# Kernel tuning notes

Measured on AMD Instinct MI355X. Metric: run time of the kernel, lower is better.

## Reference

```python
import jax, jax.numpy as jnp
import numpy as np

B, C, H, W = 4, 256, 64, 64
N = H * W


def setup_inputs() -> dict:
    key = jax.random.key(0)
    k1, k2, k3, k4, k5 = jax.random.split(key, 5)
    energy = jax.random.normal(k1, (B, N, N), dtype=jnp.float32)
    x = jax.random.normal(k2, (B, C, H, W), dtype=jnp.float32)
    # 1x1 conv params (kernel is [C_out, C_in] after squeezing the 1x1 spatial dims)
    fan = 1.0 / np.sqrt(C)
    value_w = jax.random.uniform(k3, (C, C), dtype=jnp.float32, minval=-fan, maxval=fan)
    value_b = jax.random.uniform(k4, (C,), dtype=jnp.float32, minval=-fan, maxval=fan)
    # nn.Parameter(torch.zeros(1)) -> use small random scalar so output is non-trivial
    gamma = jax.random.normal(k5, (1,), dtype=jnp.float32) * 0.1
    return {"energy": energy, "x": x, "value_w": value_w, "value_b": value_b, "gamma": gamma}


def reference(energy, x, value_w, value_b, gamma):
    # softmax over last dim of the [B, N, N] score matrix (dropout in eval mode = identity)
    attention = jax.nn.softmax(energy, axis=-1)  # [B, N, N]
    # 1x1 conv: per-pixel channel mixing
    value = jnp.einsum('bchw,oc->bohw', x, value_w) + value_b[None, :, None, None]
    value = value.reshape(x.shape[0], -1, N)  # [B, C, N]
    # out[b,c,m] = sum_n value[b,c,n] * attention[b,m,n]  (bmm with attention^T)
    out = jnp.einsum('bcn,bmn->bcm', value, attention)
    out = out.reshape(x.shape)  # [B, C, H, W]
    return gamma[0] * out + 2.0 * x
```

## Files before the change

### kernel.cpp

```cpp
#include <hip/hip_runtime.h>

#define Nn 4096
#define Cc 256
#define NN2 ((size_t)Nn * Nn)

typedef __attribute__((ext_vector_type(8))) short bf16x8;
typedef __attribute__((ext_vector_type(4))) float f32x4;

#define LDSBAR() do { \
    asm volatile("s_waitcnt lgkmcnt(0)" ::: "memory"); \
    __builtin_amdgcn_s_barrier(); \
} while (0)

__device__ __forceinline__ unsigned short f2bf(float f) {
    union { float f; unsigned u; } v; v.f = f;
    unsigned r = v.u + 0x7FFF + ((v.u >> 16) & 1);
    return (unsigned short)(r >> 16);
}

__device__ __forceinline__ bf16x8 pack2(const float4& a, const float4& b) {
    bf16x8 o;
    o[0] = (short)f2bf(a.x); o[1] = (short)f2bf(a.y);
    o[2] = (short)f2bf(a.z); o[3] = (short)f2bf(a.w);
    o[4] = (short)f2bf(b.x); o[5] = (short)f2bf(b.y);
    o[6] = (short)f2bf(b.z); o[7] = (short)f2bf(b.w);
    return o;
}

__device__ __forceinline__ void expstore(const float4& a, const float4& b,
                                         unsigned short* dst, float& sacc) {
    const float s0 = __expf(a.x), s1 = __expf(a.y), s2 = __expf(a.z), s3 = __expf(a.w);
    const float s4 = __expf(b.x), s5 = __expf(b.y), s6 = __expf(b.z), s7 = __expf(b.w);
    sacc += ((s0 + s1) + (s2 + s3)) + ((s4 + s5) + (s6 + s7));
    bf16x8 o;
    o[0] = (short)f2bf(s0); o[1] = (short)f2bf(s1);
    o[2] = (short)f2bf(s2); o[3] = (short)f2bf(s3);
    o[4] = (short)f2bf(s4); o[5] = (short)f2bf(s5);
    o[6] = (short)f2bf(s6); o[7] = (short)f2bf(s7);
    *(bf16x8*)dst = o;
}

__global__ __launch_bounds__(256) void value_gemm(
    const float* __restrict__ X, const float* __restrict__ W,
    const float* __restrict__ bias, unsigned short* __restrict__ Vout)
{
    __shared__ float Xs[256][33];

    const int t = threadIdx.x;
    const int b  = blockIdx.x >> 7;
    const int n0 = (blockIdx.x & 127) << 5;
    const int wave = t >> 6, lane = t & 63;
    const int lrow = lane & 15, lq = lane >> 4;

    const float* Xb = X + (size_t)b * Cc * Nn + n0;

    {
        const int r0 = t >> 3, c4 = (t & 7) << 2;
        #pragma unroll
        for (int i = 0; i < 8; ++i) {
            const int r = r0 + i * 32;
            const float4 v = *(const float4*)(Xb + (size_t)r * Nn + c4);
            Xs[r][c4 + 0] = v.x; Xs[r][c4 + 1] = v.y;
            Xs[r][c4 + 2] = v.z; Xs[r][c4 + 3] = v.w;
        }
    }
    __syncthreads();

    f32x4 acc[4][2] = {};

    #pragma unroll 2
    for (int k0 = 0; k0 < Cc; k0 += 32) {
        bf16x8 af[4];
        #pragma unroll
        for (int ci = 0; ci < 4; ++ci) {
            const float* wp = W + (size_t)(wave * 64 + ci * 16 + lrow) * Cc + k0 + lq * 8;
            af[ci] = pack2(*(const float4*)wp, *(const float4*)(wp + 4));
        }
        bf16x8 bp[2];
        #pragma unroll
        for (int mi = 0; mi < 2; ++mi) {
            const int n = mi * 16 + lrow;
            bf16x8 o;
            #pragma unroll
            for (int j = 0; j < 8; ++j) o[j] = (short)f2bf(Xs[k0 + lq * 8 + j][n]);
            bp[mi] = o;
        }
        #pragma unroll
        for (int ci = 0; ci < 4; ++ci)
            #pragma unroll
            for (int mi = 0; mi < 2; ++mi)
                acc[ci][mi] = __builtin_amdgcn_mfma_f32_16x16x32_bf16(
                    af[ci], bp[mi], acc[ci][mi], 0, 0, 0);
    }

    #pragma unroll
    for (int ci = 0; ci < 4; ++ci) {
        #pragma unroll
        for (int rr = 0; rr < 4; ++rr) {
            const int o = wave * 64 + ci * 16 + lq * 4 + rr;
            const float bo = bias[o];
            #pragma unroll
            for (int mi = 0; mi < 2; ++mi) {
                const int n = n0 + mi * 16 + lrow;
                Vout[((size_t)(b * Cc + o)) * Nn + n] = f2bf(acc[ci][mi][rr] + bo);
            }
        }
    }
}

__global__ __launch_bounds__(512) void attn_gemm(
    const unsigned short* __restrict__ V, const float* __restrict__ E,
    const float* __restrict__ X, const float* __restrict__ gamma,
    float* __restrict__ Out)
{
    __shared__ unsigned short Bbuf[2][64 * 64];
    __shared__ float sum_lds[64];

    const int t = threadIdx.x;
    const int blk = blockIdx.x;
    const int b  = blk & 3;
    const int m0 = (blk >> 2) << 6;

    const int wave = t >> 6, lane = t & 63;
    const int wm = wave >> 1, wn = wave & 1;
    const int lrow = lane & 15, lq = lane >> 4;
    const int l7 = lrow & 7;

    const int erow = t >> 3, eg = t & 7;
    const float* ep = E + (size_t)b * NN2 + (size_t)(m0 + erow) * Nn + eg * 8;
    unsigned short* const bst0 = &Bbuf[0][erow * 64 + ((eg ^ (erow & 7)) << 3)];
    unsigned short* const bst1 = &Bbuf[1][erow * 64 + ((eg ^ (erow & 7)) << 3)];

    const unsigned short* vbase = V + (size_t)(b * Cc + wm * 64) * Nn;
    int voff[4];
    #pragma unroll
    for (int ci = 0; ci < 4; ++ci) voff[ci] = (ci * 16 + lrow) * Nn + lq * 8;

    f32x4 acc[4][2] = {};
    float sacc = 0.f;

    float4 eA0, eA1, eB0, eB1;
    bf16x8 vA[8], vB[8];

    eA0 = *(const float4*)(ep);        eA1 = *(const float4*)(ep + 4);
    eB0 = *(const float4*)(ep + 64);   eB1 = *(const float4*)(ep + 68);
    #pragma unroll
    for (int kk = 0; kk < 2; ++kk)
        #pragma unroll
        for (int ci = 0; ci < 4; ++ci)
            vA[kk * 4 + ci] = *(const bf16x8*)(vbase + voff[ci] + kk * 32);
    expstore(eA0, eA1, bst0, sacc);
    eA0 = *(const float4*)(ep + 128);  eA1 = *(const float4*)(ep + 132);
    LDSBAR();

    for (int k = 0; k < 64; k += 2) {
        {
            bf16x8 bfr[2][2];
            #pragma unroll
            for (int kk = 0; kk < 2; ++kk)
                #pragma unroll
                for (int mi = 0; mi < 2; ++mi) {
                    const int rm = wn * 32 + mi * 16 + lrow;
                    bfr[kk][mi] = *(const bf16x8*)&Bbuf[0][rm * 64 + (((kk * 4 + lq) ^ l7) << 3)];
                }
            const int kv = (k + 1) << 6;
            #pragma unroll
            for (int kk = 0; kk < 2; ++kk)
                #pragma unroll
                for (int ci = 0; ci < 4; ++ci)
                    vB[kk * 4 + ci] = *(const bf16x8*)(vbase + voff[ci] + kv + kk * 32);
            expstore(eB0, eB1, bst1, sacc);
            const int ke = ((k + 3) & 63) << 6;
            eB0 = *(const float4*)(ep + ke); eB1 = *(const float4*)(ep + ke + 4);
            __builtin_amdgcn_s_setprio(1);
            #pragma unroll
            for (int ci = 0; ci < 4; ++ci)
                #pragma unroll
                for (int mi = 0; mi < 2; ++mi)
                    #pragma unroll
                    for (int kk = 0; kk < 2; ++kk)
                        acc[ci][mi] = __builtin_amdgcn_mfma_f32_16x16x32_bf16(
                            vA[kk * 4 + ci], bfr[kk][mi], acc[ci][mi], 0, 0, 0);
            __builtin_amdgcn_s_setprio(0);
            LDSBAR();
        }
        {
            bf16x8 bfr[2][2];
            #pragma unroll
            for (int kk = 0; kk < 2; ++kk)
                #pragma unroll
                for (int mi = 0; mi < 2; ++mi) {
                    const int rm = wn * 32 + mi * 16 + lrow;
                    bfr[kk][mi] = *(const bf16x8*)&Bbuf[1][rm * 64 + (((kk * 4 + lq) ^ l7) << 3)];
                }
            const int kv = ((k + 2) & 63) << 6;
            #pragma unroll
            for (int kk = 0; kk < 2; ++kk)
                #pragma unroll
                for (int ci = 0; ci < 4; ++ci)
                    vA[kk * 4 + ci] = *(const bf16x8*)(vbase + voff[ci] + kv + kk * 32);
            if (k != 62) {
                expstore(eA0, eA1, bst0, sacc);
                const int ke = ((k + 4) & 63) << 6;
                eA0 = *(const float4*)(ep + ke); eA1 = *(const float4*)(ep + ke + 4);
            }
            __builtin_amdgcn_s_setprio(1);
            #pragma unroll
            for (int ci = 0; ci < 4; ++ci)
                #pragma unroll
                for (int mi = 0; mi < 2; ++mi)
                    #pragma unroll
                    for (int kk = 0; kk < 2; ++kk)
                        acc[ci][mi] = __builtin_amdgcn_mfma_f32_16x16x32_bf16(
                            vB[kk * 4 + ci], bfr[kk][mi], acc[ci][mi], 0, 0, 0);
            __builtin_amdgcn_s_setprio(0);
            LDSBAR();
        }
    }

    {
        float s = sacc;
        s += __shfl_xor(s, 1);
        s += __shfl_xor(s, 2);
        s += __shfl_xor(s, 4);
        if (eg == 0) sum_lds[erow] = s;
    }
    LDSBAR();

    const float g = gamma[0];
    #pragma unroll
    for (int mi = 0; mi < 2; ++mi) {
        const int mloc = wn * 32 + mi * 16 + lrow;
        const float scale = g / sum_lds[mloc];
        const int m = m0 + mloc;
        #pragma unroll
        for (int ci = 0; ci < 4; ++ci) {
            #pragma unroll
            for (int rr = 0; rr < 4; ++rr) {
                const int c = wm * 64 + ci * 16 + lq * 4 + rr;
                const size_t off = ((size_t)(b * Cc + c)) * Nn + m;
                Out[off] = scale * acc[ci][mi][rr] + 2.0f * X[off];
            }
        }
    }
}

extern "C" void kernel_launch(void* const* d_in, const int* in_sizes, int n_in,
                              void* d_out, int out_size, void* d_ws, size_t ws_size,
                              hipStream_t stream) {
    const float* energy  = (const float*)d_in[0];
    const float* x       = (const float*)d_in[1];
    const float* value_w = (const float*)d_in[2];
    const float* value_b = (const float*)d_in[3];
    const float* gamma   = (const float*)d_in[4];
    float* out = (float*)d_out;
    unsigned short* Vws = (unsigned short*)d_ws;

    value_gemm<<<512, 256, 0, stream>>>(x, value_w, value_b, Vws);
    attn_gemm<<<256, 512, 0, stream>>>(Vws, energy, x, gamma, out);
}
```

Measured before the change: 451.3 us.

## Halve attention row tile to 32 to launch 512 blocks

The attention GEMM's m-tile shrinks from 64 rows to 32, which doubles the grid from 256 to 512 blocks so all CUs get work and more waves are resident. Each thread now loads one float4 of energy per step instead of two, and each wave computes one m-subtile instead of two. This cuts per-thread energy in flight and per-wave MFMA work per barrier. In exchange, the V matrix is re-read from global/L2 twice as often, and there is more barrier overhead relative to compute.

```diff
diff --git a/kernel.cpp b/kernel.cpp
--- a/kernel.cpp
+++ b/kernel.cpp
@@ -5,6 +5,7 @@
 #define NN2 ((size_t)Nn * Nn)
 
 typedef __attribute__((ext_vector_type(8))) short bf16x8;
+typedef __attribute__((ext_vector_type(4))) short bf16x4;
 typedef __attribute__((ext_vector_type(4))) float f32x4;
 
 #define LDSBAR() do { \
@@ -27,17 +28,14 @@
     return o;
 }
 
-__device__ __forceinline__ void expstore(const float4& a, const float4& b,
-                                         unsigned short* dst, float& sacc) {
+__device__ __forceinline__ void expstore4(const float4& a,
+                                          unsigned short* dst, float& sacc) {
     const float s0 = __expf(a.x), s1 = __expf(a.y), s2 = __expf(a.z), s3 = __expf(a.w);
-    const float s4 = __expf(b.x), s5 = __expf(b.y), s6 = __expf(b.z), s7 = __expf(b.w);
-    sacc += ((s0 + s1) + (s2 + s3)) + ((s4 + s5) + (s6 + s7));
-    bf16x8 o;
+    sacc += (s0 + s1) + (s2 + s3);
+    bf16x4 o;
     o[0] = (short)f2bf(s0); o[1] = (short)f2bf(s1);
     o[2] = (short)f2bf(s2); o[3] = (short)f2bf(s3);
-    o[4] = (short)f2bf(s4); o[5] = (short)f2bf(s5);
-    o[6] = (short)f2bf(s6); o[7] = (short)f2bf(s7);
-    *(bf16x8*)dst = o;
+    *(bf16x4*)dst = o;
 }
 
 __global__ __launch_bounds__(256) void value_gemm(
@@ -113,86 +111,81 @@
     const float* __restrict__ X, const float* __restrict__ gamma,
     float* __restrict__ Out)
 {
-    __shared__ unsigned short Bbuf[2][64 * 64];
-    __shared__ float sum_lds[64];
+    __shared__ unsigned short Bbuf[2][32 * 64];
+    __shared__ float sum_lds[32];
 
     const int t = threadIdx.x;
     const int blk = blockIdx.x;
     const int b  = blk & 3;
-    const int m0 = (blk >> 2) << 6;
+    const int m0 = (blk >> 2) << 5;
 
     const int wave = t >> 6, lane = t & 63;
     const int wm = wave >> 1, wn = wave & 1;
     const int lrow = lane & 15, lq = lane >> 4;
     const int l7 = lrow & 7;
 
-    const int erow = t >> 3, eg = t & 7;
-    const float* ep = E + (size_t)b * NN2 + (size_t)(m0 + erow) * Nn + eg * 8;
-    unsigned short* const bst0 = &Bbuf[0][erow * 64 + ((eg ^ (erow & 7)) << 3)];
-    unsigned short* const bst1 = &Bbuf[1][erow * 64 + ((eg ^ (erow & 7)) << 3)];
+    const int erow = t >> 4, eg = t & 15;
+    const float* ep = E + (size_t)b * NN2 + (size_t)(m0 + erow) * Nn + eg * 4;
+    const int ss = erow * 64 + ((((eg >> 1)) ^ (erow & 7)) << 3) + ((eg & 1) << 2);
+    unsigned short* const bst0 = &Bbuf[0][ss];
+    unsigned short* const bst1 = &Bbuf[1][ss];
 
     const unsigned short* vbase = V + (size_t)(b * Cc + wm * 64) * Nn;
     int voff[4];
     #pragma unroll
     for (int ci = 0; ci < 4; ++ci) voff[ci] = (ci * 16 + lrow) * Nn + lq * 8;
 
-    f32x4 acc[4][2] = {};
+    f32x4 acc[4] = {};
     float sacc = 0.f;
 
-    float4 eA0, eA1, eB0, eB1;
+    float4 eA, eB;
     bf16x8 vA[8], vB[8];
 
-    eA0 = *(const float4*)(ep);        eA1 = *(const float4*)(ep + 4);
-    eB0 = *(const float4*)(ep + 64);   eB1 = *(const float4*)(ep + 68);
+    eA = *(const float4*)(ep);
+    eB = *(const float4*)(ep + 64);
     #pragma unroll
     for (int kk = 0; kk < 2; ++kk)
         #pragma unroll
         for (int ci = 0; ci < 4; ++ci)
             vA[kk * 4 + ci] = *(const bf16x8*)(vbase + voff[ci] + kk * 32);
-    expstore(eA0, eA1, bst0, sacc);
-    eA0 = *(const float4*)(ep + 128);  eA1 = *(const float4*)(ep + 132);
+    expstore4(eA, bst0, sacc);
+    eA = *(const float4*)(ep + 128);
     LDSBAR();
 
     for (int k = 0; k < 64; k += 2) {
         {
-            bf16x8 bfr[2][2];
-            #pragma unroll
-            for (int kk = 0; kk < 2; ++kk)
-                #pragma unroll
-                for (int mi = 0; mi < 2; ++mi) {
-                    const int rm = wn * 32 + mi * 16 + lrow;
-                    bfr[kk][mi] = *(const bf16x8*)&Bbuf[0][rm * 64 + (((kk * 4 + lq) ^ l7) << 3)];
-                }
+            bf16x8 bfr[2];
+            #pragma unroll
+            for (int kk = 0; kk < 2; ++kk) {
+                const int rm = wn * 16 + lrow;
+                bfr[kk] = *(const bf16x8*)&Bbuf[0][rm * 64 + (((kk * 4 + lq) ^ l7) << 3)];
+            }
             const int kv = (k + 1) << 6;
             #pragma unroll
             for (int kk = 0; kk < 2; ++kk)
                 #pragma unroll
                 for (int ci = 0; ci < 4; ++ci)
                     vB[kk * 4 + ci] = *(const bf16x8*)(vbase + voff[ci] + kv + kk * 32);
-            expstore(eB0, eB1, bst1, sacc);
+            expstore4(eB, bst1, sacc);
             const int ke = ((k + 3) & 63) << 6;
-            eB0 = *(const float4*)(ep + ke); eB1 = *(const float4*)(ep + ke + 4);
+            eB = *(const float4*)(ep + ke);
             __builtin_amdgcn_s_setprio(1);
             #pragma unroll
             for (int ci = 0; ci < 4; ++ci)
                 #pragma unroll
-                for (int mi = 0; mi < 2; ++mi)
-                    #pragma unroll
-                    for (int kk = 0; kk < 2; ++kk)
-                        acc[ci][mi] = __builtin_amdgcn_mfma_f32_16x16x32_bf16(
-                            vA[kk * 4 + ci], bfr[kk][mi], acc[ci][mi], 0, 0, 0);
+                for (int kk = 0; kk < 2; ++kk)
+                    acc[ci] = __builtin_amdgcn_mfma_f32_16x16x32_bf16(
+                        vA[kk * 4 + ci], bfr[kk], acc[ci], 0, 0, 0);
             __builtin_amdgcn_s_setprio(0);
             LDSBAR();
         }
         {
-            bf16x8 bfr[2][2];
-            #pragma unroll
-            for (int kk = 0; kk < 2; ++kk)
-                #pragma unroll
-                for (int mi = 0; mi < 2; ++mi) {
-                    const int rm = wn * 32 + mi * 16 + lrow;
-                    bfr[kk][mi] = *(const bf16x8*)&Bbuf[1][rm * 64 + (((kk * 4 + lq) ^ l7) << 3)];
-                }
+            bf16x8 bfr[2];
+            #pragma unroll
+            for (int kk = 0; kk < 2; ++kk) {
+                const int rm = wn * 16 + lrow;
+                bfr[kk] = *(const bf16x8*)&Bbuf[1][rm * 64 + (((kk * 4 + lq) ^ l7) << 3)];
+            }
             const int kv = ((k + 2) & 63) << 6;
             #pragma unroll
             for (int kk = 0; kk < 2; ++kk)
@@ -200,19 +193,17 @@
                 for (int ci = 0; ci < 4; ++ci)
                     vA[kk * 4 + ci] = *(const bf16x8*)(vbase + voff[ci] + kv + kk * 32);
             if (k != 62) {
-                expstore(eA0, eA1, bst0, sacc);
+                expstore4(eA, bst0, sacc);
                 const int ke = ((k + 4) & 63) << 6;
-                eA0 = *(const float4*)(ep + ke); eA1 = *(const float4*)(ep + ke + 4);
+                eA = *(const float4*)(ep + ke);
             }
             __builtin_amdgcn_s_setprio(1);
             #pragma unroll
             for (int ci = 0; ci < 4; ++ci)
                 #pragma unroll
-                for (int mi = 0; mi < 2; ++mi)
-                    #pragma unroll
-                    for (int kk = 0; kk < 2; ++kk)
-                        acc[ci][mi] = __builtin_amdgcn_mfma_f32_16x16x32_bf16(
-                            vB[kk * 4 + ci], bfr[kk][mi], acc[ci][mi], 0, 0, 0);
+                for (int kk = 0; kk < 2; ++kk)
+                    acc[ci] = __builtin_amdgcn_mfma_f32_16x16x32_bf16(
+                        vB[kk * 4 + ci], bfr[kk], acc[ci], 0, 0, 0);
             __builtin_amdgcn_s_setprio(0);
             LDSBAR();
         }
@@ -223,14 +214,14 @@
         s += __shfl_xor(s, 1);
         s += __shfl_xor(s, 2);
         s += __shfl_xor(s, 4);
+        s += __shfl_xor(s, 8);
         if (eg == 0) sum_lds[erow] = s;
     }
     LDSBAR();
 
     const float g = gamma[0];
-    #pragma unroll
-    for (int mi = 0; mi < 2; ++mi) {
-        const int mloc = wn * 32 + mi * 16 + lrow;
+    {
+        const int mloc = wn * 16 + lrow;
         const float scale = g / sum_lds[mloc];
         const int m = m0 + mloc;
         #pragma unroll
@@ -239,7 +230,7 @@
             for (int rr = 0; rr < 4; ++rr) {
                 const int c = wm * 64 + ci * 16 + lq * 4 + rr;
                 const size_t off = ((size_t)(b * Cc + c)) * Nn + m;
-                Out[off] = scale * acc[ci][mi][rr] + 2.0f * X[off];
+                Out[off] = scale * acc[ci][rr] + 2.0f * X[off];
             }
         }
     }
@@ -257,5 +248,5 @@
     unsigned short* Vws = (unsigned short*)d_ws;
 
     value_gemm<<<512, 256, 0, stream>>>(x, value_w, value_b, Vws);
-    attn_gemm<<<256, 512, 0, stream>>>(Vws, energy, x, gamma, out);
-}
+    attn_gemm<<<512, 512, 0, stream>>>(Vws, energy, x, gamma, out);
+}
```

Result: slower. 551.5 us (+22.2%).

## Compute softmax exp directly in MFMA register layout, removing LDS staging and barriers

Applied to the files above, without the earlier changes.

The attention GEMM kernel no longer stages exponentiated energy tiles through shared memory. Each wave loads the energy elements matching its MFMA B-operand fragment, exponentiates and converts them to bf16 in registers, and feeds them straight into MFMA. Row sums are reduced with cross-lane shuffles. Blocks shrink to 256 threads covering 32 rows, with two blocks per CU, so every wave redundantly loads and exponentiates the same energy rows. V is also re-read by twice as many blocks.

```diff
diff --git a/kernel.cpp b/kernel.cpp
--- a/kernel.cpp
+++ b/kernel.cpp
@@ -6,11 +6,6 @@
 
 typedef __attribute__((ext_vector_type(8))) short bf16x8;
 typedef __attribute__((ext_vector_type(4))) float f32x4;
-
-#define LDSBAR() do { \
-    asm volatile("s_waitcnt lgkmcnt(0)" ::: "memory"); \
-    __builtin_amdgcn_s_barrier(); \
-} while (0)
 
 __device__ __forceinline__ unsigned short f2bf(float f) {
     union { float f; unsigned u; } v; v.f = f;
@@ -27,8 +22,7 @@
     return o;
 }
 
-__device__ __forceinline__ void expstore(const float4& a, const float4& b,
-                                         unsigned short* dst, float& sacc) {
+__device__ __forceinline__ bf16x8 exp8acc(const float4 a, const float4 b, float& sacc) {
     const float s0 = __expf(a.x), s1 = __expf(a.y), s2 = __expf(a.z), s3 = __expf(a.w);
     const float s4 = __expf(b.x), s5 = __expf(b.y), s6 = __expf(b.z), s7 = __expf(b.w);
     sacc += ((s0 + s1) + (s2 + s3)) + ((s4 + s5) + (s6 + s7));
@@ -37,7 +31,7 @@
     o[2] = (short)f2bf(s2); o[3] = (short)f2bf(s3);
     o[4] = (short)f2bf(s4); o[5] = (short)f2bf(s5);
     o[6] = (short)f2bf(s6); o[7] = (short)f2bf(s7);
-    *(bf16x8*)dst = o;
+    return o;
 }
 
 __global__ __launch_bounds__(256) void value_gemm(
@@ -108,138 +102,114 @@
     }
 }
 
-__global__ __launch_bounds__(512) void attn_gemm(
+__global__ __launch_bounds__(256, 2) void attn_gemm(
     const unsigned short* __restrict__ V, const float* __restrict__ E,
     const float* __restrict__ X, const float* __restrict__ gamma,
     float* __restrict__ Out)
 {
-    __shared__ unsigned short Bbuf[2][64 * 64];
-    __shared__ float sum_lds[64];
-
     const int t = threadIdx.x;
+    const int wave = t >> 6, lane = t & 63;
+    const int lrow = lane & 15, lq = lane >> 4;
     const int blk = blockIdx.x;
     const int b  = blk & 3;
-    const int m0 = (blk >> 2) << 6;
-
-    const int wave = t >> 6, lane = t & 63;
-    const int wm = wave >> 1, wn = wave & 1;
-    const int lrow = lane & 15, lq = lane >> 4;
-    const int l7 = lrow & 7;
-
-    const int erow = t >> 3, eg = t & 7;
-    const float* ep = E + (size_t)b * NN2 + (size_t)(m0 + erow) * Nn + eg * 8;
-    unsigned short* const bst0 = &Bbuf[0][erow * 64 + ((eg ^ (erow & 7)) << 3)];
-    unsigned short* const bst1 = &Bbuf[1][erow * 64 + ((eg ^ (erow & 7)) << 3)];
-
-    const unsigned short* vbase = V + (size_t)(b * Cc + wm * 64) * Nn;
+    const int m0 = (blk >> 2) << 5;
+    const int c0 = wave << 6;
+
+    const float* ep0 = E + (size_t)b * NN2 + (size_t)(m0 + lrow) * Nn + lq * 8;
+    const float* ep1 = ep0 + (size_t)16 * Nn;
+
+    const unsigned short* vbase = V + (size_t)(b * Cc + c0) * Nn;
     int voff[4];
     #pragma unroll
     for (int ci = 0; ci < 4; ++ci) voff[ci] = (ci * 16 + lrow) * Nn + lq * 8;
 
     f32x4 acc[4][2] = {};
-    float sacc = 0.f;
-
-    float4 eA0, eA1, eB0, eB1;
+    float sacc0 = 0.f, sacc1 = 0.f;
+
+    float4 eA[8], eB[8];
     bf16x8 vA[8], vB[8];
 
-    eA0 = *(const float4*)(ep);        eA1 = *(const float4*)(ep + 4);
-    eB0 = *(const float4*)(ep + 64);   eB1 = *(const float4*)(ep + 68);
+    #pragma unroll
+    for (int kk = 0; kk < 2; ++kk) {
+        eA[0 + kk * 2 + 0] = *(const float4*)(ep0 + kk * 32);
+        eA[0 + kk * 2 + 1] = *(const float4*)(ep0 + kk * 32 + 4);
+        eA[4 + kk * 2 + 0] = *(const float4*)(ep1 + kk * 32);
+        eA[4 + kk * 2 + 1] = *(const float4*)(ep1 + kk * 32 + 4);
+        eB[0 + kk * 2 + 0] = *(const float4*)(ep0 + 64 + kk * 32);
+        eB[0 + kk * 2 + 1] = *(const float4*)(ep0 + 64 + kk * 32 + 4);
+        eB[4 + kk * 2 + 0] = *(const float4*)(ep1 + 64 + kk * 32);
+        eB[4 + kk * 2 + 1] = *(const float4*)(ep1 + 64 + kk * 32 + 4);
+    }
     #pragma unroll
     for (int kk = 0; kk < 2; ++kk)
         #pragma unroll
-        for (int ci = 0; ci < 4; ++ci)
+        for (int ci = 0; ci < 4; ++ci) {
             vA[kk * 4 + ci] = *(const bf16x8*)(vbase + voff[ci] + kk * 32);
-    expstore(eA0, eA1, bst0, sacc);
-    eA0 = *(const float4*)(ep + 128);  eA1 = *(const float4*)(ep + 132);
-    LDSBAR();
-
+            vB[kk * 4 + ci] = *(const bf16x8*)(vbase + voff[ci] + 64 + kk * 32);
+        }
+
+#define HALF(Ee, Vv, ks)                                                      \
+    {                                                                          \
+        bf16x8 bfr00 = exp8acc(Ee[0], Ee[1], sacc0);              \
+        bf16x8 bfr01 = exp8acc(Ee[2], Ee[3], sacc0);              \
+        bf16x8 bfr10 = exp8acc(Ee[4], Ee[5], sacc1);              \
+        bf16x8 bfr11 = exp8acc(Ee[6], Ee[7], sacc1);              \
+        const int kc = (((ks) + 2) & 63) << 6;                                 \
+        Ee[0] = *(const float4*)(ep0 + kc);                                    \
+        Ee[1] = *(const float4*)(ep0 + kc + 4);                                \
+        Ee[2] = *(const float4*)(ep0 + kc + 32);                               \
+        Ee[3] = *(const float4*)(ep0 + kc + 36);                               \
+        Ee[4] = *(const float4*)(ep1 + kc);                                    \
+        Ee[5] = *(const float4*)(ep1 + kc + 4);                                \
+        Ee[6] = *(const float4*)(ep1 + kc + 32);                               \
+        Ee[7] = *(const float4*)(ep1 + kc + 36);                               \
+        _Pragma("unroll")                                                      \
+        for (int ci = 0; ci < 4; ++ci) {                                       \
+            acc[ci][0] = __builtin_amdgcn_mfma_f32_16x16x32_bf16(              \
+                Vv[ci], bfr00, acc[ci][0], 0, 0, 0);                           \
+            acc[ci][1] = __builtin_amdgcn_mfma_f32_16x16x32_bf16(              \
+                Vv[ci], bfr10, acc[ci][1], 0, 0, 0);                           \
+        }                                                                      \
+        _Pragma("unroll")                                                      \
+        for (int ci = 0; ci < 4; ++ci) {                                       \
+            acc[ci][0] = __builtin_amdgcn_mfma_f32_16x16x32_bf16(              \
+                Vv[4 + ci], bfr01, acc[ci][0], 0, 0, 0);                       \
+            acc[ci][1] = __builtin_amdgcn_mfma_f32_16x16x32_bf16(              \
+                Vv[4 + ci], bfr11, acc[ci][1], 0, 0, 0);                       \
+        }                                                                      \
+        _Pragma("unroll")                                                      \
+        for (int ci = 0; ci < 4; ++ci) {                                       \
+            Vv[ci]     = *(const bf16x8*)(vbase + voff[ci] + kc);              \
+            Vv[4 + ci] = *(const bf16x8*)(vbase + voff[ci] + kc + 32);         \
+        }                                                                      \
+    }
+
+    #pragma unroll 1
     for (int k = 0; k < 64; k += 2) {
-        {
-            bf16x8 bfr[2][2];
-            #pragma unroll
-            for (int kk = 0; kk < 2; ++kk)
-                #pragma unroll
-                for (int mi = 0; mi < 2; ++mi) {
-                    const int rm = wn * 32 + mi * 16 + lrow;
-                    bfr[kk][mi] = *(const bf16x8*)&Bbuf[0][rm * 64 + (((kk * 4 + lq) ^ l7) << 3)];
-                }
-            const int kv = (k + 1) << 6;
-            #pragma unroll
-            for (int kk = 0; kk < 2; ++kk)
-                #pragma unroll
-                for (int ci = 0; ci < 4; ++ci)
-                    vB[kk * 4 + ci] = *(const bf16x8*)(vbase + voff[ci] + kv + kk * 32);
-            expstore(eB0, eB1, bst1, sacc);
-            const int ke = ((k + 3) & 63) << 6;
-            eB0 = *(const float4*)(ep + ke); eB1 = *(const float4*)(ep + ke + 4);
-            __builtin_amdgcn_s_setprio(1);
-            #pragma unroll
-            for (int ci = 0; ci < 4; ++ci)
-                #pragma unroll
-                for (int mi = 0; mi < 2; ++mi)
-                    #pragma unroll
-                    for (int kk = 0; kk < 2; ++kk)
-                        acc[ci][mi] = __builtin_amdgcn_mfma_f32_16x16x32_bf16(
-                            vA[kk * 4 + ci], bfr[kk][mi], acc[ci][mi], 0, 0, 0);
-            __builtin_amdgcn_s_setprio(0);
-            LDSBAR();
-        }
-        {
-            bf16x8 bfr[2][2];
-            #pragma unroll
-            for (int kk = 0; kk < 2; ++kk)
-                #pragma unroll
-                for (int mi = 0; mi < 2; ++mi) {
-                    const int rm = wn * 32 + mi * 16 + lrow;
-                    bfr[kk][mi] = *(const bf16x8*)&Bbuf[1][rm * 64 + (((kk * 4 + lq) ^ l7) << 3)];
-                }
-            const int kv = ((k + 2) & 63) << 6;
-            #pragma unroll
-            for (int kk = 0; kk < 2; ++kk)
-                #pragma unroll
-                for (int ci = 0; ci < 4; ++ci)
-                    vA[kk * 4 + ci] = *(const bf16x8*)(vbase + voff[ci] + kv + kk * 32);
-            if (k != 62) {
-                expstore(eA0, eA1, bst0, sacc);
-                const int ke = ((k + 4) & 63) << 6;
-                eA0 = *(const float4*)(ep + ke); eA1 = *(const float4*)(ep + ke + 4);
-            }
-            __builtin_amdgcn_s_setprio(1);
-            #pragma unroll
-            for (int ci = 0; ci < 4; ++ci)
-                #pragma unroll
-                for (int mi = 0; mi < 2; ++mi)
-                    #pragma unroll
-                    for (int kk = 0; kk < 2; ++kk)
-                        acc[ci][mi] = __builtin_amdgcn_mfma_f32_16x16x32_bf16(
-                            vB[kk * 4 + ci], bfr[kk][mi], acc[ci][mi], 0, 0, 0);
-            __builtin_amdgcn_s_setprio(0);
-            LDSBAR();
-        }
-    }
-
-    {
-        float s = sacc;
-        s += __shfl_xor(s, 1);
-        s += __shfl_xor(s, 2);
-        s += __shfl_xor(s, 4);
-        if (eg == 0) sum_lds[erow] = s;
-    }
-    LDSBAR();
+        HALF(eA, vA, k);
+        HALF(eB, vB, k + 1);
+    }
+#undef HALF
+
+    float s0 = sacc0;
+    s0 += __shfl_xor(s0, 16);
+    s0 += __shfl_xor(s0, 32);
+    float s1 = sacc1;
+    s1 += __shfl_xor(s1, 16);
+    s1 += __shfl_xor(s1, 32);
 
     const float g = gamma[0];
+    const float sc[2] = { g / s0, g / s1 };
     #pragma unroll
     for (int mi = 0; mi < 2; ++mi) {
-        const int mloc = wn * 32 + mi * 16 + lrow;
-        const float scale = g / sum_lds[mloc];
-        const int m = m0 + mloc;
+        const int m = m0 + mi * 16 + lrow;
         #pragma unroll
         for (int ci = 0; ci < 4; ++ci) {
             #pragma unroll
             for (int rr = 0; rr < 4; ++rr) {
-                const int c = wm * 64 + ci * 16 + lq * 4 + rr;
+                const int c = c0 + ci * 16 + lq * 4 + rr;
                 const size_t off = ((size_t)(b * Cc + c)) * Nn + m;
-                Out[off] = scale * acc[ci][mi][rr] + 2.0f * X[off];
+                Out[off] = sc[mi] * acc[ci][mi][rr] + 2.0f * X[off];
             }
         }
     }
@@ -257,5 +227,5 @@
     unsigned short* Vws = (unsigned short*)d_ws;
 
     value_gemm<<<512, 256, 0, stream>>>(x, value_w, value_b, Vws);
-    attn_gemm<<<256, 512, 0, stream>>>(Vws, energy, x, gamma, out);
-}
+    attn_gemm<<<512, 256, 0, stream>>>(Vws, energy, x, gamma, out);
+}
```

After: 827.5 us. +83.4%, slower.

## Halve attention row tile to 32 rows and double grid for occupancy

Applied to the files above, without the earlier changes.

The attention GEMM now processes 32 query rows per block instead of 64, with 512 blocks instead of 256, so every CU gets work and more waves are resident (launch bounds request 4 waves per EU). Each wave covers 32 channels over all 32 rows, and the exp staging uses float4 per thread with an adjusted LDS swizzle. V is now re-read from global/L2 twice as often across blocks, and per-wave MFMA work per barrier is halved, adding sync overhead relative to compute.

```diff
diff --git a/kernel.cpp b/kernel.cpp
--- a/kernel.cpp
+++ b/kernel.cpp
@@ -5,6 +5,7 @@
 #define NN2 ((size_t)Nn * Nn)
 
 typedef __attribute__((ext_vector_type(8))) short bf16x8;
+typedef __attribute__((ext_vector_type(4))) short bf16x4;
 typedef __attribute__((ext_vector_type(4))) float f32x4;
 
 #define LDSBAR() do { \
@@ -27,17 +28,14 @@
     return o;
 }
 
-__device__ __forceinline__ void expstore(const float4& a, const float4& b,
-                                         unsigned short* dst, float& sacc) {
+__device__ __forceinline__ void expstore4(const float4& a,
+                                          unsigned short* dst, float& sacc) {
     const float s0 = __expf(a.x), s1 = __expf(a.y), s2 = __expf(a.z), s3 = __expf(a.w);
-    const float s4 = __expf(b.x), s5 = __expf(b.y), s6 = __expf(b.z), s7 = __expf(b.w);
-    sacc += ((s0 + s1) + (s2 + s3)) + ((s4 + s5) + (s6 + s7));
-    bf16x8 o;
+    sacc += (s0 + s1) + (s2 + s3);
+    bf16x4 o;
     o[0] = (short)f2bf(s0); o[1] = (short)f2bf(s1);
     o[2] = (short)f2bf(s2); o[3] = (short)f2bf(s3);
-    o[4] = (short)f2bf(s4); o[5] = (short)f2bf(s5);
-    o[6] = (short)f2bf(s6); o[7] = (short)f2bf(s7);
-    *(bf16x8*)dst = o;
+    *(bf16x4*)dst = o;
 }
 
 __global__ __launch_bounds__(256) void value_gemm(
@@ -108,49 +106,48 @@
     }
 }
 
-__global__ __launch_bounds__(512) void attn_gemm(
+__global__ __launch_bounds__(512, 4) void attn_gemm(
     const unsigned short* __restrict__ V, const float* __restrict__ E,
     const float* __restrict__ X, const float* __restrict__ gamma,
     float* __restrict__ Out)
 {
-    __shared__ unsigned short Bbuf[2][64 * 64];
-    __shared__ float sum_lds[64];
+    __shared__ unsigned short Bexp[2][32 * 64];
+    __shared__ float sum_lds[32];
 
     const int t = threadIdx.x;
-    const int blk = blockIdx.x;
-    const int b  = blk & 3;
-    const int m0 = (blk >> 2) << 6;
-
     const int wave = t >> 6, lane = t & 63;
-    const int wm = wave >> 1, wn = wave & 1;
     const int lrow = lane & 15, lq = lane >> 4;
     const int l7 = lrow & 7;
-
-    const int erow = t >> 3, eg = t & 7;
-    const float* ep = E + (size_t)b * NN2 + (size_t)(m0 + erow) * Nn + eg * 8;
-    unsigned short* const bst0 = &Bbuf[0][erow * 64 + ((eg ^ (erow & 7)) << 3)];
-    unsigned short* const bst1 = &Bbuf[1][erow * 64 + ((eg ^ (erow & 7)) << 3)];
-
-    const unsigned short* vbase = V + (size_t)(b * Cc + wm * 64) * Nn;
-    int voff[4];
-    #pragma unroll
-    for (int ci = 0; ci < 4; ++ci) voff[ci] = (ci * 16 + lrow) * Nn + lq * 8;
-
-    f32x4 acc[4][2] = {};
+    const int blk = blockIdx.x;
+    const int b  = (blk & 7) >> 1;
+    const int m0 = (((blk >> 3) << 1) | (blk & 1)) << 5;
+
+    const int erow = t >> 4, eg = t & 15;
+    const float* ep = E + (size_t)b * NN2 + (size_t)(m0 + erow) * Nn + eg * 4;
+    const int ss = erow * 64 + (((eg >> 1) ^ (erow & 7)) << 3) + ((eg & 1) << 2);
+    unsigned short* const bst0 = &Bexp[0][ss];
+    unsigned short* const bst1 = &Bexp[1][ss];
+
+    const unsigned short* vbase = V + (size_t)(b * Cc + wave * 32) * Nn;
+    int voff[2];
+    voff[0] = lrow * Nn + lq * 8;
+    voff[1] = (16 + lrow) * Nn + lq * 8;
+
+    f32x4 acc[2][2] = {};
     float sacc = 0.f;
 
-    float4 eA0, eA1, eB0, eB1;
-    bf16x8 vA[8], vB[8];
-
-    eA0 = *(const float4*)(ep);        eA1 = *(const float4*)(ep + 4);
-    eB0 = *(const float4*)(ep + 64);   eB1 = *(const float4*)(ep + 68);
+    float4 eE0, eE1;
+    bf16x8 vA[4], vB[4];
+
+    eE0 = *(const float4*)(ep);
+    eE1 = *(const float4*)(ep + 64);
     #pragma unroll
     for (int kk = 0; kk < 2; ++kk)
         #pragma unroll
-        for (int ci = 0; ci < 4; ++ci)
-            vA[kk * 4 + ci] = *(const bf16x8*)(vbase + voff[ci] + kk * 32);
-    expstore(eA0, eA1, bst0, sacc);
-    eA0 = *(const float4*)(ep + 128);  eA1 = *(const float4*)(ep + 132);
+        for (int ci = 0; ci < 2; ++ci)
+            vA[kk * 2 + ci] = *(const bf16x8*)(vbase + voff[ci] + kk * 32);
+    expstore4(eE0, bst0, sacc);
+    eE0 = *(const float4*)(ep + 128);
     LDSBAR();
 
     for (int k = 0; k < 64; k += 2) {
@@ -160,27 +157,26 @@
             for (int kk = 0; kk < 2; ++kk)
                 #pragma unroll
                 for (int mi = 0; mi < 2; ++mi) {
-                    const int rm = wn * 32 + mi * 16 + lrow;
-                    bfr[kk][mi] = *(const bf16x8*)&Bbuf[0][rm * 64 + (((kk * 4 + lq) ^ l7) << 3)];
+                    const int rm = mi * 16 + lrow;
+                    bfr[kk][mi] = *(const bf16x8*)&Bexp[0][rm * 64 + (((kk * 4 + lq) ^ l7) << 3)];
                 }
             const int kv = (k + 1) << 6;
             #pragma unroll
             for (int kk = 0; kk < 2; ++kk)
                 #pragma unroll
-                for (int ci = 0; ci < 4; ++ci)
-                    vB[kk * 4 + ci] = *(const bf16x8*)(vbase + voff[ci] + kv + kk * 32);
-            expstore(eB0, eB1, bst1, sacc);
-            const int ke = ((k + 3) & 63) << 6;
-            eB0 = *(const float4*)(ep + ke); eB1 = *(const float4*)(ep + ke + 4);
+                for (int ci = 0; ci < 2; ++ci)
+                    vB[kk * 2 + ci] = *(const bf16x8*)(vbase + voff[ci] + kv + kk * 32);
+            expstore4(eE1, bst1, sacc);
+            eE1 = *(const float4*)(ep + (((k + 3) & 63) << 6));
             __builtin_amdgcn_s_setprio(1);
             #pragma unroll
-            for (int ci = 0; ci < 4; ++ci)
+            for (int ci = 0; ci < 2; ++ci)
                 #pragma unroll
                 for (int mi = 0; mi < 2; ++mi)
                     #pragma unroll
                     for (int kk = 0; kk < 2; ++kk)
                         acc[ci][mi] = __builtin_amdgcn_mfma_f32_16x16x32_bf16(
-                            vA[kk * 4 + ci], bfr[kk][mi], acc[ci][mi], 0, 0, 0);
+                            vA[kk * 2 + ci], bfr[kk][mi], acc[ci][mi], 0, 0, 0);
             __builtin_amdgcn_s_setprio(0);
             LDSBAR();
         }
@@ -190,29 +186,28 @@
             for (int kk = 0; kk < 2; ++kk)
                 #pragma unroll
                 for (int mi = 0; mi < 2; ++mi) {
-                    const int rm = wn * 32 + mi * 16 + lrow;
-                    bfr[kk][mi] = *(const bf16x8*)&Bbuf[1][rm * 64 + (((kk * 4 + lq) ^ l7) << 3)];
+                    const int rm = mi * 16 + lrow;
+                    bfr[kk][mi] = *(const bf16x8*)&Bexp[1][rm * 64 + (((kk * 4 + lq) ^ l7) << 3)];
                 }
             const int kv = ((k + 2) & 63) << 6;
             #pragma unroll
             for (int kk = 0; kk < 2; ++kk)
                 #pragma unroll
-                for (int ci = 0; ci < 4; ++ci)
-                    vA[kk * 4 + ci] = *(const bf16x8*)(vbase + voff[ci] + kv + kk * 32);
+                for (int ci = 0; ci < 2; ++ci)
+                    vA[kk * 2 + ci] = *(const bf16x8*)(vbase + voff[ci] + kv + kk * 32);
             if (k != 62) {
-                expstore(eA0, eA1, bst0, sacc);
-                const int ke = ((k + 4) & 63) << 6;
-                eA0 = *(const float4*)(ep + ke); eA1 = *(const float4*)(ep + ke + 4);
+                expstore4(eE0, bst0, sacc);
+                eE0 = *(const float4*)(ep + (((k + 4) & 63) << 6));
             }
             __builtin_amdgcn_s_setprio(1);
             #pragma unroll
-            for (int ci = 0; ci < 4; ++ci)
+            for (int ci = 0; ci < 2; ++ci)
                 #pragma unroll
                 for (int mi = 0; mi < 2; ++mi)
                     #pragma unroll
                     for (int kk = 0; kk < 2; ++kk)
                         acc[ci][mi] = __builtin_amdgcn_mfma_f32_16x16x32_bf16(
-                            vB[kk * 4 + ci], bfr[kk][mi], acc[ci][mi], 0, 0, 0);
+                            vB[kk * 2 + ci], bfr[kk][mi], acc[ci][mi], 0, 0, 0);
             __builtin_amdgcn_s_setprio(0);
             LDSBAR();
         }
@@ -223,21 +218,22 @@
         s += __shfl_xor(s, 1);
         s += __shfl_xor(s, 2);
         s += __shfl_xor(s, 4);
+        s += __shfl_xor(s, 8);
         if (eg == 0) sum_lds[erow] = s;
     }
-    LDSBAR();
+    __syncthreads();
 
     const float g = gamma[0];
     #pragma unroll
     for (int mi = 0; mi < 2; ++mi) {
-        const int mloc = wn * 32 + mi * 16 + lrow;
+        const int mloc = mi * 16 + lrow;
         const float scale = g / sum_lds[mloc];
         const int m = m0 + mloc;
         #pragma unroll
-        for (int ci = 0; ci < 4; ++ci) {
+        for (int ci = 0; ci < 2; ++ci) {
             #pragma unroll
             for (int rr = 0; rr < 4; ++rr) {
-                const int c = wm * 64 + ci * 16 + lq * 4 + rr;
+                const int c = wave * 32 + ci * 16 + lq * 4 + rr;
                 const size_t off = ((size_t)(b * Cc + c)) * Nn + m;
                 Out[off] = scale * acc[ci][mi][rr] + 2.0f * X[off];
             }
@@ -257,5 +253,5 @@
     unsigned short* Vws = (unsigned short*)d_ws;
 
     value_gemm<<<512, 256, 0, stream>>>(x, value_w, value_b, Vws);
-    attn_gemm<<<256, 512, 0, stream>>>(Vws, energy, x, gamma, out);
-}
+    attn_gemm<<<512, 512, 0, stream>>>(Vws, energy, x, gamma, out);
+}
```

After: 455.3 us. No clear change (+0.9%).
